# Performance work log

Measured on AMD Instinct MI355X. Metric: run time of the kernel, lower is better.

The kernel has to match this reference:

```python
import jax, jax.numpy as jnp
import numpy as np

B, T, D, H, L, F = 32, 512, 1024, 1024, 2, 256  # batch, time, input dim, units, layers, feature_size


def setup_inputs() -> dict:
    key = jax.random.key(0)
    ks = jax.random.split(key, 9)
    s_in = 1.0 / np.sqrt(D)
    s_h = 1.0 / np.sqrt(H)
    x = jax.random.normal(ks[0], (B, T, D), dtype=jnp.float32)
    # Stacked LSTM params: gate order [i, f, g, o] concatenated along last axis.
    Wx = jax.random.normal(ks[1], (L, D, 4 * H), dtype=jnp.float32) * s_in
    Wh = jax.random.normal(ks[2], (L, H, 4 * H), dtype=jnp.float32) * s_h
    b = jnp.zeros((L, 4 * H), dtype=jnp.float32)
    # Output heads.
    Wmu = jax.random.normal(ks[3], (H, F), dtype=jnp.float32) * s_h
    bmu = jnp.zeros((F,), dtype=jnp.float32)
    Wls = jax.random.normal(ks[4], (H, F), dtype=jnp.float32) * s_h
    bls = jnp.zeros((F,), dtype=jnp.float32)
    y_min = jnp.zeros((F,), dtype=jnp.float32)  # y_min init arg (0.0 broadcast)
    return {"x": x, "Wx": Wx, "Wh": Wh, "b": b, "Wmu": Wmu, "bmu": bmu,
            "Wls": Wls, "bls": bls, "y_min": y_min}


def _lstm_layer(x, Wx, Wh, b):
    # x: [B, T, Din]; Wx: [Din, 4H]; Wh: [H, 4H]; b: [4H]
    Bn = x.shape[0]
    Hn = Wh.shape[0]
    # Precompute input projections for all timesteps (one big GEMM).
    x_proj = jnp.einsum('btd,dg->btg', x, Wx) + b  # [B, T, 4H]

    def step(carry, xp):
        h, c = carry
        g = xp + h @ Wh  # [B, 4H]
        i, f, gg, o = jnp.split(g, 4, axis=-1)
        c = jax.nn.sigmoid(f) * c + jax.nn.sigmoid(i) * jnp.tanh(gg)
        h = jax.nn.sigmoid(o) * jnp.tanh(c)
        return (h, c), h

    h0 = jnp.zeros((Bn, Hn), dtype=x.dtype)
    c0 = jnp.zeros((Bn, Hn), dtype=x.dtype)
    _, hs = jax.lax.scan(step, (h0, c0), jnp.swapaxes(x_proj, 0, 1))  # hs: [T, B, H]
    return jnp.swapaxes(hs, 0, 1)  # [B, T, H]


def reference(x, Wx, Wh, b, Wmu, bmu, Wls, bls, y_min):
    for l in range(Wx.shape[0]):  # small fixed n_layers loop
        x = _lstm_layer(x, Wx[l], Wh[l], b[l])
    mu = jax.nn.softplus(x @ Wmu + bmu) + y_min  # [B, T, F]
    log_sigma = x @ Wls + bls                    # [B, T, F]
    return (mu, log_sigma)
```

## Files before the change

kernel.cpp:

```cpp
#include <hip/hip_runtime.h>

typedef unsigned short u16;
typedef unsigned int   u32;
typedef unsigned long long u64;
typedef short s16x4 __attribute__((ext_vector_type(4)));
typedef short s16x8 __attribute__((ext_vector_type(8)));
typedef float f32x4 __attribute__((ext_vector_type(4)));
typedef u32   u32x4 __attribute__((ext_vector_type(4)));

#define GK 1024

__device__ inline u16 f2bf(float f) {
    u32 u = __builtin_bit_cast(u32, f);
    u += 0x7FFFu + ((u >> 16) & 1u);
    return (u16)(u >> 16);
}
__device__ inline u16 f2h(float f) {
    _Float16 h = (_Float16)f;
    return __builtin_bit_cast(u16, h);
}
__device__ inline float h2f(u16 u) {
    return (float)__builtin_bit_cast(_Float16, u);
}
__device__ inline float fast_sigmoid(float x) {
    return __builtin_amdgcn_rcpf(1.f + __expf(-x));
}
__device__ inline float fast_tanh(float x) {
    return 1.f - 2.f * __builtin_amdgcn_rcpf(1.f + __expf(2.f * x));
}
__device__ inline f32x4 mfma16(s16x8 a, s16x8 b, f32x4 c) {
    return __builtin_amdgcn_mfma_f32_16x16x32_bf16(a, b, c, 0, 0, 0);
}
__device__ inline s16x8 mk8(s16x4 lo, s16x4 hi) {
    return __builtin_shufflevector(lo, hi, 0, 1, 2, 3, 4, 5, 6, 7);
}

__global__ void k_f2bf(const float* __restrict__ in, u16* __restrict__ out, int n) {
    int i = (blockIdx.x * 256 + threadIdx.x) * 4;
    if (i < n) {
        float4 v = *(const float4*)(in + i);
        ushort4 o;
        o.x = f2bf(v.x); o.y = f2bf(v.y); o.z = f2bf(v.z); o.w = f2bf(v.w);
        *(ushort4*)(out + i) = o;
    }
}

__global__ void k_transpose_bf(const float* __restrict__ in, u16* __restrict__ out,
                               int R, int C) {
    __shared__ float tile[32][33];
    int tid = threadIdx.x;
    int xs = (tid & 7) * 4;
    int y  = tid >> 3;
    int r0 = blockIdx.y * 32, c0 = blockIdx.x * 32;
    float4 v = *(const float4*)(in + (size_t)(r0 + y) * C + c0 + xs);
    tile[y][xs + 0] = v.x; tile[y][xs + 1] = v.y;
    tile[y][xs + 2] = v.z; tile[y][xs + 3] = v.w;
    __syncthreads();
    ushort4 o;
    o.x = f2bf(tile[xs + 0][y]); o.y = f2bf(tile[xs + 1][y]);
    o.z = f2bf(tile[xs + 2][y]); o.w = f2bf(tile[xs + 3][y]);
    *(ushort4*)(out + (size_t)(c0 + y) * R + r0 + xs) = o;
}

template<int MODE>
__launch_bounds__(256, 2)
__global__ void k_gemm(const u16* __restrict__ A, const u16* __restrict__ BT,
                       const float* __restrict__ bias,
                       u16* __restrict__ Cb, float* __restrict__ Cf,
                       const float* __restrict__ b2, const float* __restrict__ ymin,
                       int gridN) {
    int bid = blockIdx.x;
    int m0 = (bid / gridN) * 128, n0 = (bid % gridN) * 128;
    __shared__ u16 As[128 * 40];
    __shared__ u16 Bs[128 * 40];
    int tid = threadIdx.x;
    int lane = tid & 63, w = tid >> 6;
    int wr = w >> 1, wc = w & 1;
    int rr = lane & 15, r16 = lane >> 4;
    f32x4 acc[4][4] = {};
    for (int kt = 0; kt < GK / 32; ++kt) {
        int k0 = kt * 32;
#pragma unroll
        for (int it = 0; it < 2; ++it) {
            int idx = it * 256 + tid;
            int row = idx >> 2, ch = idx & 3;
            if (MODE == 0) {
                *(u32x4*)(&As[row * 40 + ch * 8]) =
                    *(const u32x4*)(A + (size_t)(m0 + row) * GK + k0 + ch * 8);
            } else {
                int m = m0 + row;
                size_t aaddr = (size_t)(m >> 5) * 32768 + (size_t)((k0 >> 3) + ch) * 256
                             + (size_t)(m & 31) * 8;
                *(u32x4*)(&As[row * 40 + ch * 8]) = *(const u32x4*)(A + aaddr);
            }
            *(u32x4*)(&Bs[row * 40 + ch * 8]) =
                *(const u32x4*)(BT + (size_t)(n0 + row) * GK + k0 + ch * 8);
        }
        __syncthreads();
        s16x8 af[4], bfr[4];
#pragma unroll
        for (int i = 0; i < 4; ++i) {
            int abase = (wr * 64 + i * 16 + rr) * 40 + r16 * 4;
            af[i] = mk8(*(const s16x4*)(&As[abase]), *(const s16x4*)(&As[abase + 16]));
            int bbase = (wc * 64 + i * 16 + rr) * 40 + r16 * 4;
            bfr[i] = mk8(*(const s16x4*)(&Bs[bbase]), *(const s16x4*)(&Bs[bbase + 16]));
        }
#pragma unroll
        for (int i = 0; i < 4; ++i)
#pragma unroll
            for (int j = 0; j < 4; ++j)
                acc[i][j] = mfma16(af[i], bfr[j], acc[i][j]);
        __syncthreads();
    }
#pragma unroll
    for (int i = 0; i < 4; ++i) {
#pragma unroll
        for (int j = 0; j < 4; ++j) {
#pragma unroll
            for (int r = 0; r < 4; ++r) {
                int m = m0 + wr * 64 + i * 16 + r16 * 4 + r;
                int n = n0 + wc * 64 + j * 16 + rr;
                float v = acc[i][j][r];
                if (MODE == 0) {
                    v += bias[n];
                    int orow = (m & 511) * 32 + (m >> 9);
                    int colx = ((n & 1023) << 2) | (n >> 10);
                    Cb[(size_t)orow * 4096 + colx] = f2h(v);
                } else {
                    int orow = (m & 31) * 512 + (m >> 5);
                    if (n < 256) {
                        v += bias[n];
                        float sp = fmaxf(v, 0.f) + log1pf(expf(-fabsf(v)));
                        Cf[(size_t)orow * 256 + n] = sp + ymin[n];
                    } else {
                        v += b2[n - 256];
                        Cf[4194304 + (size_t)orow * 256 + (n - 256)] = v;
                    }
                }
            }
        }
    }
}

__launch_bounds__(512, 2)
__global__ void k_fused(const u16* __restrict__ Wh0T, const u16* __restrict__ Wx1T,
                        const u16* __restrict__ Wh1T, const u16* __restrict__ xproj,
                        const float* __restrict__ b1,
                        u16* __restrict__ hseq0, u16* __restrict__ hseq1,
                        u32* __restrict__ flags) {
    __shared__ float part[4][64][4];
    int tid = threadIdx.x, blk = blockIdx.x;
    int lane = tid & 63, w = tid >> 6;
    int grp = w >> 2, wl = w & 3;
    int mt = wl >> 1, nt = wl & 1;
    int u0 = blk * 8;
    int rr = lane & 15, r16 = lane >> 4;

    int cg = (rr & 3) * 1024 + u0 + nt * 4 + (rr >> 2);
    const u16* wstat = (grp == 0 ? Wh0T : Wh1T) + (size_t)cg * GK + r16 * 4;
    u64 wpx_u = (u64)(uintptr_t)(Wx1T + (size_t)cg * GK + r16 * 4);
    s16x8 bstat[32];
#pragma unroll
    for (int q = 0; q < 32; ++q)
        bstat[q] = mk8(*(const s16x4*)(wstat + q * 32),
                       *(const s16x4*)(wstat + q * 32 + 16));

    int b_    = mt * 16 + (lane >> 4) * 4 + (lane & 3);
    int u_loc = nt * 4 + ((lane >> 2) & 3);
    int unit  = u0 + u_loc;
    float c0 = 0.f, c1 = 0.f;
    float b1r[4];
#pragma unroll
    for (int g = 0; g < 4; ++g) b1r[g] = b1[g * 1024 + unit];

    const u16* xp = xproj + (size_t)b_ * 4096 + (size_t)unit * 4;
    const int boff = (mt * 16 + rr) * 8 + (r16 & 1) * 4;
    const int kq   = (r16 >> 1);
    const int soff = blk * 256 + b_ * 8 + nt * 4;

    for (int r = 0; r <= 512; ++r) {
        u32 tgt = (u32)r;
        while (true) {
            u32 v0 = __hip_atomic_load(&flags[lane], __ATOMIC_RELAXED,
                                       __HIP_MEMORY_SCOPE_AGENT);
            u32 v1 = __hip_atomic_load(&flags[64 + lane], __ATOMIC_RELAXED,
                                       __HIP_MEMORY_SCOPE_AGENT);
            if (__all((v0 >= tgt) & (v1 >= tgt))) break;
            __builtin_amdgcn_s_sleep(1);
        }
        __builtin_amdgcn_sched_barrier(0);

        f32x4 aE = {}, aO = {}, xE = {}, xO = {};
        u64 xv = 0;
        if (grp == 0) {
            if (r < 512) xv = *(const u64*)(xp + (size_t)r * 131072);
            asm volatile("" : "+v"(wpx_u));
            const u16* wpx = (const u16*)(uintptr_t)wpx_u;
            const u16* h0p = hseq0 + (size_t)r * 32768 + boff;
#pragma unroll
            for (int c = 0; c < 4; ++c) {
                u64 lo8[8], hi8[8];
                s16x8 bx[8];
#pragma unroll
                for (int j = 0; j < 8; ++j) {
                    int q = c * 8 + j;
                    lo8[j] = __hip_atomic_load((const u64*)(h0p + (q * 4 + kq) * 256),
                                               __ATOMIC_RELAXED, __HIP_MEMORY_SCOPE_AGENT);
                    hi8[j] = __hip_atomic_load((const u64*)(h0p + (q * 4 + kq + 2) * 256),
                                               __ATOMIC_RELAXED, __HIP_MEMORY_SCOPE_AGENT);
                    bx[j] = mk8(*(const s16x4*)(wpx + q * 32),
                                *(const s16x4*)(wpx + q * 32 + 16));
                }
#pragma unroll
                for (int j = 0; j < 8; ++j) {
                    int q = c * 8 + j;
                    s16x8 a = mk8(__builtin_bit_cast(s16x4, lo8[j]),
                                  __builtin_bit_cast(s16x4, hi8[j]));
                    if (q & 1) { aO = mfma16(a, bstat[q], aO); xO = mfma16(a, bx[j], xO); }
                    else       { aE = mfma16(a, bstat[q], aE); xE = mfma16(a, bx[j], xE); }
                }
            }
        } else {
            if (r > 0) {
                const u16* h1p = hseq1 + (size_t)(r - 1) * 32768 + boff;
#pragma unroll
                for (int c = 0; c < 4; ++c) {
                    u64 lo8[8], hi8[8];
#pragma unroll
                    for (int j = 0; j < 8; ++j) {
                        int q = c * 8 + j;
                        lo8[j] = __hip_atomic_load((const u64*)(h1p + (q * 4 + kq) * 256),
                                                   __ATOMIC_RELAXED, __HIP_MEMORY_SCOPE_AGENT);
                        hi8[j] = __hip_atomic_load((const u64*)(h1p + (q * 4 + kq + 2) * 256),
                                                   __ATOMIC_RELAXED, __HIP_MEMORY_SCOPE_AGENT);
                    }
#pragma unroll
                    for (int j = 0; j < 8; ++j) {
                        int q = c * 8 + j;
                        s16x8 a = mk8(__builtin_bit_cast(s16x4, lo8[j]),
                                      __builtin_bit_cast(s16x4, hi8[j]));
                        if (q & 1) aO = mfma16(a, bstat[q], aO);
                        else       aE = mfma16(a, bstat[q], aE);
                    }
                }
            }
            *(f32x4*)(&part[wl][lane][0]) = aE + aO;
        }
        __syncthreads();

        if (grp == 0) {
            if (r < 512) {
                f32x4 acc = aE + aO;
                float r0 = acc[0], r1 = acc[1], r2 = acc[2], r3 = acc[3];
                float x0 = __shfl_xor(r0, 1), x1 = __shfl_xor(r1, 1);
                float x2 = __shfl_xor(r2, 1), x3 = __shfl_xor(r3, 1);
                bool o1 = lane & 1;
                float s0 = o1 ? x1 : r0, s1 = o1 ? r1 : x0;
                float s2 = o1 ? x3 : r2, s3 = o1 ? r3 : x2;
                float y0 = __shfl_xor(s0, 2), y1 = __shfl_xor(s1, 2);
                float y2 = __shfl_xor(s2, 2), y3 = __shfl_xor(s3, 2);
                bool o2 = lane & 2;
                float gi = (o2 ? y2 : s0) + h2f((u16)(xv));
                float gf = (o2 ? y3 : s1) + h2f((u16)(xv >> 16));
                float gg = (o2 ? s2 : y0) + h2f((u16)(xv >> 32));
                float go = (o2 ? s3 : y1) + h2f((u16)(xv >> 48));
                float I  = fast_sigmoid(gi);
                float Fg = fast_sigmoid(gf);
                float G  = fast_tanh(gg);
                float O  = fast_sigmoid(go);
                c0 = Fg * c0 + I * G;
                u32 hq = (u32)f2bf(O * fast_tanh(c0));
                u32 o4 = (u32)__shfl_xor((int)hq, 4);
                u32 m32 = (lane & 4) ? ((o4 & 0xffffu) | (hq << 16))
                                     : ((hq & 0xffffu) | (o4 << 16));
                u32 o8 = (u32)__shfl_xor((int)m32, 8);
                u64 m64 = (lane & 8) ? (((u64)o8) | ((u64)m32 << 32))
                                     : (((u64)m32) | ((u64)o8 << 32));
                if ((lane & 12) == 0)
                    __hip_atomic_store((u64*)(hseq0 + (size_t)(r + 1) * 32768 + soff),
                                       m64, __ATOMIC_RELAXED, __HIP_MEMORY_SCOPE_AGENT);
            }
            if (r > 0) {
                f32x4 acc = xE + xO + *(const f32x4*)(&part[wl][lane][0]);
                float r0 = acc[0], r1 = acc[1], r2 = acc[2], r3 = acc[3];
                float x0 = __shfl_xor(r0, 1), x1 = __shfl_xor(r1, 1);
                float x2 = __shfl_xor(r2, 1), x3 = __shfl_xor(r3, 1);
                bool o1 = lane & 1;
                float s0 = o1 ? x1 : r0, s1 = o1 ? r1 : x0;
                float s2 = o1 ? x3 : r2, s3 = o1 ? r3 : x2;
                float y0 = __shfl_xor(s0, 2), y1 = __shfl_xor(s1, 2);
                float y2 = __shfl_xor(s2, 2), y3 = __shfl_xor(s3, 2);
                bool o2 = lane & 2;
                float gi = (o2 ? y2 : s0) + b1r[0];
                float gf = (o2 ? y3 : s1) + b1r[1];
                float gg = (o2 ? s2 : y0) + b1r[2];
                float go = (o2 ? s3 : y1) + b1r[3];
                float I  = fast_sigmoid(gi);
                float Fg = fast_sigmoid(gf);
                float G  = fast_tanh(gg);
                float O  = fast_sigmoid(go);
                c1 = Fg * c1 + I * G;
                u32 hq = (u32)f2bf(O * fast_tanh(c1));
                u32 o4 = (u32)__shfl_xor((int)hq, 4);
                u32 m32 = (lane & 4) ? ((o4 & 0xffffu) | (hq << 16))
                                     : ((hq & 0xffffu) | (o4 << 16));
                u32 o8 = (u32)__shfl_xor((int)m32, 8);
                u64 m64 = (lane & 8) ? (((u64)o8) | ((u64)m32 << 32))
                                     : (((u64)m32) | ((u64)o8 << 32));
                if ((lane & 12) == 0)
                    __hip_atomic_store((u64*)(hseq1 + (size_t)r * 32768 + soff),
                                       m64, __ATOMIC_RELAXED, __HIP_MEMORY_SCOPE_AGENT);
            }
        }
        __syncthreads();
        if (tid == 0)
            __hip_atomic_store(&flags[blk], (u32)(r + 1), __ATOMIC_RELAXED,
                               __HIP_MEMORY_SCOPE_AGENT);
    }
}

extern "C" void kernel_launch(void* const* d_in, const int* in_sizes, int n_in,
                              void* d_out, int out_size, void* d_ws, size_t ws_size,
                              hipStream_t stream) {
    const float* x   = (const float*)d_in[0];
    const float* Wx  = (const float*)d_in[1];
    const float* Wh  = (const float*)d_in[2];
    const float* b   = (const float*)d_in[3];
    const float* Wmu = (const float*)d_in[4];
    const float* bmu = (const float*)d_in[5];
    const float* Wls = (const float*)d_in[6];
    const float* bls = (const float*)d_in[7];
    const float* ym  = (const float*)d_in[8];
    float* out = (float*)d_out;

    char* ws = (char*)d_ws;
    u16* hseq0 = (u16*)(ws);
    u16* xbf   = (u16*)(ws);
    u16* hseq1 = (u16*)(ws + 33619968);
    u16* wxT   = (u16*)(ws + 67239936);
    u16* whT   = (u16*)(ws + 84017152);
    u16* whdT  = (u16*)(ws + 100794368);
    u16* xproj = (u16*)(ws + 101842944);
    u32* flags = (u32*)(ws + 236060672);

    k_f2bf<<<16384, 256, 0, stream>>>(x, xbf, 16777216);
    dim3 tg(128, 32);
    k_transpose_bf<<<tg, 256, 0, stream>>>(Wx,           wxT,           1024, 4096);
    k_transpose_bf<<<tg, 256, 0, stream>>>(Wx + 4194304, wxT + 4194304, 1024, 4096);
    k_transpose_bf<<<tg, 256, 0, stream>>>(Wh,           whT,           1024, 4096);
    k_transpose_bf<<<tg, 256, 0, stream>>>(Wh + 4194304, whT + 4194304, 1024, 4096);
    dim3 hg(8, 32);
    k_transpose_bf<<<hg, 256, 0, stream>>>(Wmu, whdT,          1024, 256);
    k_transpose_bf<<<hg, 256, 0, stream>>>(Wls, whdT + 262144, 1024, 256);

    k_gemm<0><<<4096, 256, 0, stream>>>(xbf, wxT, b, xproj, nullptr, nullptr, nullptr, 32);

    hipMemsetAsync(hseq0, 0, 65536, stream);
    hipMemsetAsync(hseq1, 0, 65536, stream);
    hipMemsetAsync(flags, 0, 512, stream);

    k_fused<<<128, 512, 0, stream>>>(whT, wxT + 4194304, whT + 4194304, xproj,
                                     b + 4096, hseq0, hseq1, flags);

    k_gemm<1><<<512, 256, 0, stream>>>(hseq1 + 32768, whdT, bmu, nullptr, out,
                                       bls, ym, 4);
}
```

Baseline: 8.161 ms.

## Stage recurrent weights in LDS and poll flags from one wave

```diff
diff --git a/kernel.cpp b/kernel.cpp
--- a/kernel.cpp
+++ b/kernel.cpp
@@ -148,6 +148,7 @@
                         const float* __restrict__ b1,
                         u16* __restrict__ hseq0, u16* __restrict__ hseq1,
                         u32* __restrict__ flags) {
+    __shared__ u16 wlds[2][32][128][8];
     __shared__ float part[4][64][4];
     int tid = threadIdx.x, blk = blockIdx.x;
     int lane = tid & 63, w = tid >> 6;
@@ -157,13 +158,16 @@
     int rr = lane & 15, r16 = lane >> 4;
 
     int cg = (rr & 3) * 1024 + u0 + nt * 4 + (rr >> 2);
-    const u16* wstat = (grp == 0 ? Wh0T : Wh1T) + (size_t)cg * GK + r16 * 4;
+    if (wl < 2) {
+        const u16* wsrc = (grp == 0 ? Wh0T : Wh1T) + (size_t)cg * GK + r16 * 4;
+#pragma unroll
+        for (int q = 0; q < 32; ++q) {
+            s16x8 f = mk8(*(const s16x4*)(wsrc + q * 32),
+                          *(const s16x4*)(wsrc + q * 32 + 16));
+            *(s16x8*)(&wlds[grp][q][nt * 64 + lane][0]) = f;
+        }
+    }
     u64 wpx_u = (u64)(uintptr_t)(Wx1T + (size_t)cg * GK + r16 * 4);
-    s16x8 bstat[32];
-#pragma unroll
-    for (int q = 0; q < 32; ++q)
-        bstat[q] = mk8(*(const s16x4*)(wstat + q * 32),
-                       *(const s16x4*)(wstat + q * 32 + 16));
 
     int b_    = mt * 16 + (lane >> 4) * 4 + (lane & 3);
     int u_loc = nt * 4 + ((lane >> 2) & 3);
@@ -177,18 +181,23 @@
     const int boff = (mt * 16 + rr) * 8 + (r16 & 1) * 4;
     const int kq   = (r16 >> 1);
     const int soff = blk * 256 + b_ * 8 + nt * 4;
+    const u16* wq = &wlds[grp][0][nt * 64 + lane][0];
+
+    __syncthreads();
 
     for (int r = 0; r <= 512; ++r) {
-        u32 tgt = (u32)r;
-        while (true) {
-            u32 v0 = __hip_atomic_load(&flags[lane], __ATOMIC_RELAXED,
-                                       __HIP_MEMORY_SCOPE_AGENT);
-            u32 v1 = __hip_atomic_load(&flags[64 + lane], __ATOMIC_RELAXED,
-                                       __HIP_MEMORY_SCOPE_AGENT);
-            if (__all((v0 >= tgt) & (v1 >= tgt))) break;
-            __builtin_amdgcn_s_sleep(1);
-        }
-        __builtin_amdgcn_sched_barrier(0);
+        if (w == 0) {
+            u32 tgt = (u32)r;
+            while (true) {
+                u32 v0 = __hip_atomic_load(&flags[lane], __ATOMIC_RELAXED,
+                                           __HIP_MEMORY_SCOPE_AGENT);
+                u32 v1 = __hip_atomic_load(&flags[64 + lane], __ATOMIC_RELAXED,
+                                           __HIP_MEMORY_SCOPE_AGENT);
+                if (__all((v0 >= tgt) & (v1 >= tgt))) break;
+                __builtin_amdgcn_s_sleep(1);
+            }
+        }
+        __syncthreads();
 
         f32x4 aE = {}, aO = {}, xE = {}, xO = {};
         u64 xv = 0;
@@ -216,8 +225,9 @@
                     int q = c * 8 + j;
                     s16x8 a = mk8(__builtin_bit_cast(s16x4, lo8[j]),
                                   __builtin_bit_cast(s16x4, hi8[j]));
-                    if (q & 1) { aO = mfma16(a, bstat[q], aO); xO = mfma16(a, bx[j], xO); }
-                    else       { aE = mfma16(a, bstat[q], aE); xE = mfma16(a, bx[j], xE); }
+                    s16x8 bw = *(const s16x8*)(wq + (size_t)q * 1024);
+                    if (q & 1) { aO = mfma16(a, bw, aO); xO = mfma16(a, bx[j], xO); }
+                    else       { aE = mfma16(a, bw, aE); xE = mfma16(a, bx[j], xE); }
                 }
             }
         } else {
@@ -239,8 +249,9 @@
                         int q = c * 8 + j;
                         s16x8 a = mk8(__builtin_bit_cast(s16x4, lo8[j]),
                                       __builtin_bit_cast(s16x4, hi8[j]));
-                        if (q & 1) aO = mfma16(a, bstat[q], aO);
-                        else       aE = mfma16(a, bstat[q], aE);
+                        s16x8 bw = *(const s16x8*)(wq + (size_t)q * 1024);
+                        if (q & 1) aO = mfma16(a, bw, aO);
+                        else       aE = mfma16(a, bw, aE);
                     }
                 }
             }
```

Measured after the change: 8.023 ms. No clear change (-1.7%).

## Replace global flag barrier with per-element sentinel polling in persistent LSTM kernel

Applied to the files above, without the earlier changes.

```diff
diff --git a/kernel.cpp b/kernel.cpp
--- a/kernel.cpp
+++ b/kernel.cpp
@@ -9,6 +9,7 @@
 typedef u32   u32x4 __attribute__((ext_vector_type(4)));
 
 #define GK 1024
+#define P64 0x7F7F7F7F7F7F7F7FULL
 
 __device__ inline u16 f2bf(float f) {
     u32 u = __builtin_bit_cast(u32, f);
@@ -33,6 +34,17 @@
 }
 __device__ inline s16x8 mk8(s16x4 lo, s16x4 hi) {
     return __builtin_shufflevector(lo, hi, 0, 1, 2, 3, 4, 5, 6, 7);
+}
+__device__ inline u64 aload(const u16* p) {
+    return __hip_atomic_load((const u64*)p, __ATOMIC_RELAXED, __HIP_MEMORY_SCOPE_AGENT);
+}
+__device__ inline u64 spin_ok(u64 v, const u16* p) {
+    int guard = 0;
+    while (v == P64 && ++guard < (1 << 22)) {
+        __builtin_amdgcn_s_sleep(1);
+        v = aload(p);
+    }
+    return v;
 }
 
 __global__ void k_f2bf(const float* __restrict__ in, u16* __restrict__ out, int n) {
@@ -87,14 +99,17 @@
             if (MODE == 0) {
                 *(u32x4*)(&As[row * 40 + ch * 8]) =
                     *(const u32x4*)(A + (size_t)(m0 + row) * GK + k0 + ch * 8);
+                *(u32x4*)(&Bs[row * 40 + ch * 8]) =
+                    *(const u32x4*)(BT + (size_t)(n0 + row) * GK + k0 + ch * 8);
             } else {
                 int m = m0 + row;
-                size_t aaddr = (size_t)(m >> 5) * 32768 + (size_t)((k0 >> 3) + ch) * 256
-                             + (size_t)(m & 31) * 8;
+                size_t aaddr = (size_t)(m >> 5) * 32768 + (size_t)(m & 31) * 1024
+                             + k0 + ch * 8;
                 *(u32x4*)(&As[row * 40 + ch * 8]) = *(const u32x4*)(A + aaddr);
-            }
-            *(u32x4*)(&Bs[row * 40 + ch * 8]) =
-                *(const u32x4*)(BT + (size_t)(n0 + row) * GK + k0 + ch * 8);
+                const u16* bp = BT + (size_t)(n0 + row) * GK + k0 + ch * 4;
+                *(s16x8*)(&Bs[row * 40 + ch * 8]) =
+                    mk8(*(const s16x4*)bp, *(const s16x4*)(bp + 16));
+            }
         }
         __syncthreads();
         s16x8 af[4], bfr[4];
@@ -142,115 +157,114 @@
     }
 }
 
-__launch_bounds__(512, 2)
+__launch_bounds__(512, 1)
 __global__ void k_fused(const u16* __restrict__ Wh0T, const u16* __restrict__ Wx1T,
                         const u16* __restrict__ Wh1T, const u16* __restrict__ xproj,
                         const float* __restrict__ b1,
-                        u16* __restrict__ hseq0, u16* __restrict__ hseq1,
-                        u32* __restrict__ flags) {
-    __shared__ float part[4][64][4];
+                        u16* __restrict__ hseq0, u16* __restrict__ hseq1) {
+    __shared__ u16 wlds[2][32][2][64][8];
+    __shared__ f32x4 part[2][2][4][64];
     int tid = threadIdx.x, blk = blockIdx.x;
     int lane = tid & 63, w = tid >> 6;
     int grp = w >> 2, wl = w & 3;
-    int mt = wl >> 1, nt = wl & 1;
-    int u0 = blk * 8;
+    int mt = wl >> 1, qh = wl & 1;
     int rr = lane & 15, r16 = lane >> 4;
-
-    int cg = (rr & 3) * 1024 + u0 + nt * 4 + (rr >> 2);
-    const u16* wstat = (grp == 0 ? Wh0T : Wh1T) + (size_t)cg * GK + r16 * 4;
-    u64 wpx_u = (u64)(uintptr_t)(Wx1T + (size_t)cg * GK + r16 * 4);
-    s16x8 bstat[32];
-#pragma unroll
-    for (int q = 0; q < 32; ++q)
-        bstat[q] = mk8(*(const s16x4*)(wstat + q * 32),
-                       *(const s16x4*)(wstat + q * 32 + 16));
-
-    int b_    = mt * 16 + (lane >> 4) * 4 + (lane & 3);
-    int u_loc = nt * 4 + ((lane >> 2) & 3);
-    int unit  = u0 + u_loc;
+    int g32 = blk >> 2, sub = blk & 3;
+
+    {
+        const u16* WT = (grp == 0) ? Wh0T : Wh1T;
+#pragma unroll
+        for (int qq = 0; qq < 8; ++qq) {
+            int q = wl * 8 + qq;
+#pragma unroll
+            for (int ct = 0; ct < 2; ++ct) {
+                int unit = g32 * 32 + sub * 4 + (rr >> 2) + ct * 16;
+                const u16* src = WT + (size_t)((rr & 3) * 1024 + unit) * GK + q * 32 + r16 * 4;
+                *(s16x8*)(&wlds[grp][q][ct][lane][0]) =
+                    mk8(*(const s16x4*)src, *(const s16x4*)(src + 16));
+            }
+        }
+    }
+
+    int b_ = mt * 16 + (lane >> 4) * 4 + (lane & 3);
+    int unitE = g32 * 32 + sub * 4 + ((lane >> 2) & 3) + qh * 16;
     float c0 = 0.f, c1 = 0.f;
     float b1r[4];
 #pragma unroll
-    for (int g = 0; g < 4; ++g) b1r[g] = b1[g * 1024 + unit];
-
-    const u16* xp = xproj + (size_t)b_ * 4096 + (size_t)unit * 4;
-    const int boff = (mt * 16 + rr) * 8 + (r16 & 1) * 4;
-    const int kq   = (r16 >> 1);
-    const int soff = blk * 256 + b_ * 8 + nt * 4;
+    for (int g = 0; g < 4; ++g) b1r[g] = b1[g * 1024 + unitE];
+    const u16* xp = xproj + (size_t)b_ * 4096 + (size_t)unitE * 4;
+    const int soff = b_ * 1024 + g32 * 32 + sub * 8 + qh * 4;
+    const int cbase = (mt * 16 + rr) * 1024 + qh * 512 + r16 * 8;
+
+    u64 wpx_u = (u64)(uintptr_t)(Wx1T +
+        (size_t)((rr & 3) * 1024 + g32 * 32 + sub * 4 + (rr >> 2)) * GK + r16 * 4);
+
+    __syncthreads();
 
     for (int r = 0; r <= 512; ++r) {
-        u32 tgt = (u32)r;
-        while (true) {
-            u32 v0 = __hip_atomic_load(&flags[lane], __ATOMIC_RELAXED,
-                                       __HIP_MEMORY_SCOPE_AGENT);
-            u32 v1 = __hip_atomic_load(&flags[64 + lane], __ATOMIC_RELAXED,
-                                       __HIP_MEMORY_SCOPE_AGENT);
-            if (__all((v0 >= tgt) & (v1 >= tgt))) break;
-            __builtin_amdgcn_s_sleep(1);
-        }
-        __builtin_amdgcn_sched_barrier(0);
-
-        f32x4 aE = {}, aO = {}, xE = {}, xO = {};
+        f32x4 a0[2] = {}, a1[2] = {};
         u64 xv = 0;
         if (grp == 0) {
             if (r < 512) xv = *(const u64*)(xp + (size_t)r * 131072);
             asm volatile("" : "+v"(wpx_u));
             const u16* wpx = (const u16*)(uintptr_t)wpx_u;
-            const u16* h0p = hseq0 + (size_t)r * 32768 + boff;
-#pragma unroll
-            for (int c = 0; c < 4; ++c) {
-                u64 lo8[8], hi8[8];
-                s16x8 bx[8];
-#pragma unroll
-                for (int j = 0; j < 8; ++j) {
-                    int q = c * 8 + j;
-                    lo8[j] = __hip_atomic_load((const u64*)(h0p + (q * 4 + kq) * 256),
-                                               __ATOMIC_RELAXED, __HIP_MEMORY_SCOPE_AGENT);
-                    hi8[j] = __hip_atomic_load((const u64*)(h0p + (q * 4 + kq + 2) * 256),
-                                               __ATOMIC_RELAXED, __HIP_MEMORY_SCOPE_AGENT);
-                    bx[j] = mk8(*(const s16x4*)(wpx + q * 32),
-                                *(const s16x4*)(wpx + q * 32 + 16));
-                }
-#pragma unroll
-                for (int j = 0; j < 8; ++j) {
-                    int q = c * 8 + j;
-                    s16x8 a = mk8(__builtin_bit_cast(s16x4, lo8[j]),
-                                  __builtin_bit_cast(s16x4, hi8[j]));
-                    if (q & 1) { aO = mfma16(a, bstat[q], aO); xO = mfma16(a, bx[j], xO); }
-                    else       { aE = mfma16(a, bstat[q], aE); xE = mfma16(a, bx[j], xE); }
-                }
-            }
+            const u16* hp = hseq0 + (size_t)r * 32768 + cbase;
+            u64 lo[16], hi[16];
+#pragma unroll
+            for (int j = 0; j < 16; ++j) {
+                lo[j] = aload(hp + j * 32);
+                hi[j] = aload(hp + j * 32 + 4);
+            }
+#pragma unroll
+            for (int j = 0; j < 16; ++j) {
+                lo[j] = spin_ok(lo[j], hp + j * 32);
+                hi[j] = spin_ok(hi[j], hp + j * 32 + 4);
+                s16x8 a = mk8(__builtin_bit_cast(s16x4, lo[j]),
+                              __builtin_bit_cast(s16x4, hi[j]));
+                int q = qh * 16 + j;
+                s16x8 bw0 = *(const s16x8*)(&wlds[0][q][0][lane][0]);
+                s16x8 bw1 = *(const s16x8*)(&wlds[0][q][1][lane][0]);
+                const u16* bp = wpx + q * 32;
+                s16x8 bx0 = mk8(*(const s16x4*)bp, *(const s16x4*)(bp + 16));
+                s16x8 bx1 = mk8(*(const s16x4*)(bp + 16384),
+                                *(const s16x4*)(bp + 16384 + 16));
+                a0[0] = mfma16(a, bw0, a0[0]);
+                a0[1] = mfma16(a, bw1, a0[1]);
+                a1[0] = mfma16(a, bx0, a1[0]);
+                a1[1] = mfma16(a, bx1, a1[1]);
+            }
+            part[mt][1 - qh][0][lane] = a0[1 - qh];
+            part[mt][1 - qh][1][lane] = a1[1 - qh];
         } else {
             if (r > 0) {
-                const u16* h1p = hseq1 + (size_t)(r - 1) * 32768 + boff;
-#pragma unroll
-                for (int c = 0; c < 4; ++c) {
-                    u64 lo8[8], hi8[8];
-#pragma unroll
-                    for (int j = 0; j < 8; ++j) {
-                        int q = c * 8 + j;
-                        lo8[j] = __hip_atomic_load((const u64*)(h1p + (q * 4 + kq) * 256),
-                                                   __ATOMIC_RELAXED, __HIP_MEMORY_SCOPE_AGENT);
-                        hi8[j] = __hip_atomic_load((const u64*)(h1p + (q * 4 + kq + 2) * 256),
-                                                   __ATOMIC_RELAXED, __HIP_MEMORY_SCOPE_AGENT);
-                    }
-#pragma unroll
-                    for (int j = 0; j < 8; ++j) {
-                        int q = c * 8 + j;
-                        s16x8 a = mk8(__builtin_bit_cast(s16x4, lo8[j]),
-                                      __builtin_bit_cast(s16x4, hi8[j]));
-                        if (q & 1) aO = mfma16(a, bstat[q], aO);
-                        else       aE = mfma16(a, bstat[q], aE);
-                    }
+                const u16* hp = hseq1 + (size_t)(r - 1) * 32768 + cbase;
+                u64 lo[16], hi[16];
+#pragma unroll
+                for (int j = 0; j < 16; ++j) {
+                    lo[j] = aload(hp + j * 32);
+                    hi[j] = aload(hp + j * 32 + 4);
                 }
-            }
-            *(f32x4*)(&part[wl][lane][0]) = aE + aO;
+#pragma unroll
+                for (int j = 0; j < 16; ++j) {
+                    lo[j] = spin_ok(lo[j], hp + j * 32);
+                    hi[j] = spin_ok(hi[j], hp + j * 32 + 4);
+                    s16x8 a = mk8(__builtin_bit_cast(s16x4, lo[j]),
+                                  __builtin_bit_cast(s16x4, hi[j]));
+                    int q = qh * 16 + j;
+                    s16x8 bw0 = *(const s16x8*)(&wlds[1][q][0][lane][0]);
+                    s16x8 bw1 = *(const s16x8*)(&wlds[1][q][1][lane][0]);
+                    a0[0] = mfma16(a, bw0, a0[0]);
+                    a0[1] = mfma16(a, bw1, a0[1]);
+                }
+            }
+            part[mt][0][2 + qh][lane] = a0[0];
+            part[mt][1][2 + qh][lane] = a0[1];
         }
         __syncthreads();
 
         if (grp == 0) {
             if (r < 512) {
-                f32x4 acc = aE + aO;
+                f32x4 acc = a0[qh] + part[mt][qh][0][lane];
                 float r0 = acc[0], r1 = acc[1], r2 = acc[2], r3 = acc[3];
                 float x0 = __shfl_xor(r0, 1), x1 = __shfl_xor(r1, 1);
                 float x2 = __shfl_xor(r2, 1), x3 = __shfl_xor(r3, 1);
@@ -281,7 +295,8 @@
                                        m64, __ATOMIC_RELAXED, __HIP_MEMORY_SCOPE_AGENT);
             }
             if (r > 0) {
-                f32x4 acc = xE + xO + *(const f32x4*)(&part[wl][lane][0]);
+                f32x4 acc = a1[qh] + part[mt][qh][1][lane]
+                          + part[mt][qh][2][lane] + part[mt][qh][3][lane];
                 float r0 = acc[0], r1 = acc[1], r2 = acc[2], r3 = acc[3];
                 float x0 = __shfl_xor(r0, 1), x1 = __shfl_xor(r1, 1);
                 float x2 = __shfl_xor(r2, 1), x3 = __shfl_xor(r3, 1);
@@ -313,9 +328,6 @@
             }
         }
         __syncthreads();
-        if (tid == 0)
-            __hip_atomic_store(&flags[blk], (u32)(r + 1), __ATOMIC_RELAXED,
-                               __HIP_MEMORY_SCOPE_AGENT);
     }
 }
 
@@ -341,7 +353,9 @@
     u16* whT   = (u16*)(ws + 84017152);
     u16* whdT  = (u16*)(ws + 100794368);
     u16* xproj = (u16*)(ws + 101842944);
-    u32* flags = (u32*)(ws + 236060672);
+
+    hipMemsetAsync(hseq1, 0, 65536, stream);
+    hipMemsetAsync(hseq1 + 32768, 0x7F, 33619968 - 65536, stream);
 
     k_f2bf<<<16384, 256, 0, stream>>>(x, xbf, 16777216);
     dim3 tg(128, 32);
@@ -356,11 +370,10 @@
     k_gemm<0><<<4096, 256, 0, stream>>>(xbf, wxT, b, xproj, nullptr, nullptr, nullptr, 32);
 
     hipMemsetAsync(hseq0, 0, 65536, stream);
-    hipMemsetAsync(hseq1, 0, 65536, stream);
-    hipMemsetAsync(flags, 0, 512, stream);
+    hipMemsetAsync(hseq0 + 32768, 0x7F, 33619968 - 65536, stream);
 
     k_fused<<<128, 512, 0, stream>>>(whT, wxT + 4194304, whT + 4194304, xproj,
-                                     b + 4096, hseq0, hseq1, flags);
+                                     b + 4096, hseq0, hseq1);
 
     k_gemm<1><<<512, 256, 0, stream>>>(hseq1 + 32768, whdT, bmu, nullptr, out,
                                        bls, ym, 4);
```

Result: slower. 9.685 ms (+18.7%).
